# Kernel optimization log

Measured on AMD Instinct MI355X. Metric: run time of the kernel, lower is better.

Reference implementation:

```python
import jax, jax.numpy as jnp
import numpy as np

VOCAB_SIZE = 8192
DIM = 64


def setup_inputs() -> dict:
    key = jax.random.key(0)
    k1, k2 = jax.random.split(key)
    patches = jax.random.normal(k1, (16, 2048, DIM), dtype=jnp.float32)
    vocab = jax.random.normal(k2, (VOCAB_SIZE, DIM), dtype=jnp.float32)
    return {"patches": patches, "vocab": vocab}


def reference(patches, vocab):
    # torch.cdist(patches, vocab) -> [B, N, K] euclidean distances, then argmin over K.
    # argmin is invariant under sqrt, so compare squared distances:
    x2 = jnp.sum(patches * patches, axis=-1, keepdims=True)       # [B, N, 1]
    c2 = jnp.sum(vocab * vocab, axis=-1)                           # [K]
    xc = jnp.einsum("bnd,kd->bnk", patches, vocab)                # [B, N, K]
    d2 = x2 - 2.0 * xc + c2                                        # [B, N, K]
    tokens = jnp.argmin(d2, axis=-1)                               # [B, N] int
    return tokens
```

## Files before the change

### kernel.cpp

```cpp
#include <hip/hip_runtime.h>
#include <float.h>

#define VOCAB 8192
#define DIM 64
#define NQ 32768
#define CHUNK 64
#define THREADS 256
#define QPB 256
#define NSLICE 4

typedef __attribute__((ext_vector_type(8))) _Float16 half8;
typedef __attribute__((ext_vector_type(4))) float f32x4;

#define LO_SCALE 4096.0f
#define LO_INV   2.44140625e-4f

__global__ __launch_bounds__(256) void c2_kernel(const float* __restrict__ vocab,
                                                 float* __restrict__ c2h) {
    int c = blockIdx.x * 256 + threadIdx.x;
    const float4* row = (const float4*)(vocab + (size_t)c * DIM);
    float a0 = 0.f, a1 = 0.f, a2 = 0.f, a3 = 0.f;
#pragma unroll
    for (int k = 0; k < DIM / 4; ++k) {
        float4 v = row[k];
        a0 = fmaf(v.x, v.x, a0); a1 = fmaf(v.y, v.y, a1);
        a2 = fmaf(v.z, v.z, a2); a3 = fmaf(v.w, v.w, a3);
    }
    c2h[c] = -0.5f * ((a0 + a1) + (a2 + a3));
}

__global__ __launch_bounds__(256) void split_kernel(const float* __restrict__ src,
                                                    _Float16* __restrict__ hi,
                                                    _Float16* __restrict__ lo) {
    int t = blockIdx.x * 256 + threadIdx.x;
    const float4* s = (const float4*)(src + (size_t)t * 8);
    float4 f0 = s[0], f1 = s[1];
    float x[8] = {f0.x, f0.y, f0.z, f0.w, f1.x, f1.y, f1.z, f1.w};
    half8 h, l;
#pragma unroll
    for (int j = 0; j < 8; ++j) {
        _Float16 hh = (_Float16)x[j];
        h[j] = hh;
        l[j] = (_Float16)((x[j] - (float)hh) * LO_SCALE);
    }
    *(half8*)(hi + (size_t)t * 8) = h;
    *(half8*)(lo + (size_t)t * 8) = l;
}

__device__ __forceinline__ void gload_lds16(const void* g, void* lds_dst) {
    __builtin_amdgcn_global_load_lds(
        (const __attribute__((address_space(1))) void*)g,
        (__attribute__((address_space(3))) void*)lds_dst, 16, 0, 0);
}
__device__ __forceinline__ void gload_lds4(const void* g, void* lds_dst) {
    __builtin_amdgcn_global_load_lds(
        (const __attribute__((address_space(1))) void*)g,
        (__attribute__((address_space(3))) void*)lds_dst, 4, 0, 0);
}

__global__ __launch_bounds__(THREADS, 2)
void argmin_mfma(const float* __restrict__ patches,
                 const _Float16* __restrict__ vhi,
                 const _Float16* __restrict__ vlo,
                 const float* __restrict__ c2g,
                 float* __restrict__ ws_best,
                 int*   __restrict__ ws_idx) {
    constexpr int CSLICE = VOCAB / NSLICE;
    constexpr int NCHUNK = CSLICE / CHUNK;
    __shared__ __align__(16) char smem[2 * 16384 + 2 * 256];

    const int tid   = threadIdx.x;
    const int lane  = tid & 63;
    const int w     = tid >> 6;
    const int slice = blockIdx.x & (NSLICE - 1);
    const int qg    = blockIdx.x / NSLICE;
    const int qbase = qg * QPB + w * 64;
    const int cbase = slice * CSLICE;

    const int arow = lane & 15;
    const int akc  = lane >> 4;
    half8 Ah[4][2], Al[4][2];
#pragma unroll
    for (int t = 0; t < 4; ++t)
#pragma unroll
        for (int ks = 0; ks < 2; ++ks) {
            const float* p = patches + (size_t)(qbase + t * 16 + arow) * DIM
                           + ks * 32 + akc * 8;
            float4 f0 = *(const float4*)p;
            float4 f1 = *(const float4*)(p + 4);
            float x[8] = {f0.x, f0.y, f0.z, f0.w, f1.x, f1.y, f1.z, f1.w};
            half8 h, l;
#pragma unroll
            for (int j = 0; j < 8; ++j) {
                _Float16 hh = (_Float16)x[j];
                h[j] = hh;
                l[j] = (_Float16)((x[j] - (float)hh) * LO_SCALE);
            }
            Ah[t][ks] = h; Al[t][ks] = l;
        }

    const int s_srcoff = ((lane >> 3) * DIM) + (((lane & 7) ^ (lane >> 3)) * 8);
    const int fr = lane & 15;
    const int fx = fr & 7;
    const int b_off0 = fr * 128 + (((0 * 4 + akc) ^ fx) * 16);
    const int b_off1 = fr * 128 + (((1 * 4 + akc) ^ fx) * 16);

    auto stage = [&](int ch, int buf) {
        const size_t crow = (size_t)(cbase + ch * CHUNK) * DIM;
        char* dst = smem + buf * 16384;
#pragma unroll
        for (int j = 0; j < 2; ++j) {
            int r0 = (w + 4 * j) * 8;
            gload_lds16(vhi + crow + (size_t)r0 * DIM + s_srcoff, dst + r0 * 128);
            gload_lds16(vlo + crow + (size_t)r0 * DIM + s_srcoff, dst + 8192 + r0 * 128);
        }
        gload_lds4(c2g + cbase + ch * CHUNK + lane, smem + 32768 + buf * 256);
    };

    float best[4][4];
    int   bidx[4][4];
#pragma unroll
    for (int t = 0; t < 4; ++t)
#pragma unroll
        for (int j = 0; j < 4; ++j) { best[t][j] = -FLT_MAX; bidx[t][j] = 0; }

    stage(0, 0);

    for (int ch = 0; ch < NCHUNK; ++ch) {
        const int cur = ch & 1;
        if (ch + 1 < NCHUNK) {
            stage(ch + 1, cur ^ 1);
            asm volatile("s_waitcnt vmcnt(5)" ::: "memory");
        } else {
            asm volatile("s_waitcnt vmcnt(0)" ::: "memory");
        }
        __builtin_amdgcn_s_barrier();

        const char*  hib = smem + cur * 16384;
        const char*  lob = hib + 8192;
        const float* c2b = (const float*)(smem + 32768 + cur * 256);
        const int cb = cbase + ch * CHUNK;

#pragma unroll
        for (int nt = 0; nt < 4; ++nt) {
            const int rt = nt * 16;
            half8 Bh0 = *(const half8*)(hib + rt * 128 + b_off0);
            half8 Bh1 = *(const half8*)(hib + rt * 128 + b_off1);
            half8 Bl0 = *(const half8*)(lob + rt * 128 + b_off0);
            half8 Bl1 = *(const half8*)(lob + rt * 128 + b_off1);
            const float c2h = c2b[rt + fr];
            const int  cidx = cb + rt + fr;
            __builtin_amdgcn_s_setprio(1);
#pragma unroll
            for (int t = 0; t < 4; ++t) {
                f32x4 am = {c2h, c2h, c2h, c2h};
                f32x4 al = {0.f, 0.f, 0.f, 0.f};
                am = __builtin_amdgcn_mfma_f32_16x16x32_f16(Ah[t][0], Bh0, am, 0, 0, 0);
                am = __builtin_amdgcn_mfma_f32_16x16x32_f16(Ah[t][1], Bh1, am, 0, 0, 0);
                al = __builtin_amdgcn_mfma_f32_16x16x32_f16(Ah[t][0], Bl0, al, 0, 0, 0);
                al = __builtin_amdgcn_mfma_f32_16x16x32_f16(Ah[t][1], Bl1, al, 0, 0, 0);
                al = __builtin_amdgcn_mfma_f32_16x16x32_f16(Al[t][0], Bh0, al, 0, 0, 0);
                al = __builtin_amdgcn_mfma_f32_16x16x32_f16(Al[t][1], Bh1, al, 0, 0, 0);
#pragma unroll
                for (int j = 0; j < 4; ++j) {
                    float val = fmaf(al[j], LO_INV, am[j]);
                    if (val > best[t][j]) { best[t][j] = val; bidx[t][j] = cidx; }
                }
            }
            __builtin_amdgcn_s_setprio(0);
        }
        __builtin_amdgcn_s_barrier();
    }

#pragma unroll
    for (int t = 0; t < 4; ++t)
#pragma unroll
        for (int j = 0; j < 4; ++j) {
            float b = best[t][j]; int bi = bidx[t][j];
#pragma unroll
            for (int d = 1; d < 16; d <<= 1) {
                float ob = __shfl_xor(b, d, 64);
                int   oi = __shfl_xor(bi, d, 64);
                if (ob > b || (ob == b && oi < bi)) { b = ob; bi = oi; }
            }
            best[t][j] = b; bidx[t][j] = bi;
        }

    if ((lane & 15) == 0) {
        const int rg = lane >> 4;
#pragma unroll
        for (int t = 0; t < 4; ++t)
#pragma unroll
            for (int j = 0; j < 4; ++j) {
                int q = qbase + t * 16 + rg * 4 + j;
                ws_best[(size_t)slice * NQ + q] = best[t][j];
                ws_idx [(size_t)slice * NQ + q] = bidx[t][j];
            }
    }
}

__global__ __launch_bounds__(256) void merge_kernel(const float* __restrict__ ws_best,
                                                    const int* __restrict__ ws_idx,
                                                    int* __restrict__ out) {
    int q = blockIdx.x * 256 + threadIdx.x;
    float b = ws_best[q]; int bi = ws_idx[q];
#pragma unroll
    for (int s = 1; s < NSLICE; ++s) {
        float v = ws_best[(size_t)s * NQ + q];
        int  vi = ws_idx[(size_t)s * NQ + q];
        if (v > b || (v == b && vi < bi)) { b = v; bi = vi; }
    }
    out[q] = bi;
}

extern "C" void kernel_launch(void* const* d_in, const int* in_sizes, int n_in,
                              void* d_out, int out_size, void* d_ws, size_t ws_size,
                              hipStream_t stream) {
    const float* patches = (const float*)d_in[0];
    const float* vocab   = (const float*)d_in[1];
    char* ws = (char*)d_ws;
    float*    c2    = (float*)ws;
    _Float16* vhi   = (_Float16*)(ws + 32768);
    _Float16* vlo   = (_Float16*)(ws + 32768 + 1048576);
    float*    wbest = (float*)(ws + 32768 + 2097152);
    int*      widx  = (int*)  (ws + 32768 + 2097152 + 524288);
    int* out = (int*)d_out;

    c2_kernel   <<<VOCAB / 256, 256, 0, stream>>>(vocab, c2);
    split_kernel<<<(VOCAB * DIM / 8) / 256, 256, 0, stream>>>(vocab, vhi, vlo);
    argmin_mfma <<<(NQ / QPB) * NSLICE, THREADS, 0, stream>>>(patches, vhi, vlo, c2, wbest, widx);
    merge_kernel<<<NQ / 256, 256, 0, stream>>>(wbest, widx, out);
}
```

Measured before the change: 103.9 us.

## Switch distance GEMM to 32x32x16 MFMA tiles with new LDS layout

Replaces the 16x16x32 MFMA tiling with 32x32x16 MFMA, so each wave handles 32 queries against 32-codeword tiles. The LDS staging layout and read offsets change to feed the new B fragment shape. The argmin update now runs once per 16-element accumulator after the K loop. Queries per block drop from 256 to 128, which doubles the grid and the re-staging of the vocabulary across blocks. The per-block compare work and the cross-lane reduction widen to 32 lanes.

```diff
diff --git a/kernel.cpp b/kernel.cpp
--- a/kernel.cpp
+++ b/kernel.cpp
@@ -6,11 +6,11 @@
 #define NQ 32768
 #define CHUNK 64
 #define THREADS 256
-#define QPB 256
+#define QPB 128
 #define NSLICE 4
 
 typedef __attribute__((ext_vector_type(8))) _Float16 half8;
-typedef __attribute__((ext_vector_type(4))) float f32x4;
+typedef __attribute__((ext_vector_type(16))) float f32x16;
 
 #define LO_SCALE 4096.0f
 #define LO_INV   2.44140625e-4f
@@ -74,55 +74,53 @@
     const int w     = tid >> 6;
     const int slice = blockIdx.x & (NSLICE - 1);
     const int qg    = blockIdx.x / NSLICE;
-    const int qbase = qg * QPB + w * 64;
+    const int qbase = qg * QPB + w * 32;
     const int cbase = slice * CSLICE;
 
-    const int arow = lane & 15;
-    const int akc  = lane >> 4;
-    half8 Ah[4][2], Al[4][2];
-#pragma unroll
-    for (int t = 0; t < 4; ++t)
-#pragma unroll
-        for (int ks = 0; ks < 2; ++ks) {
-            const float* p = patches + (size_t)(qbase + t * 16 + arow) * DIM
-                           + ks * 32 + akc * 8;
-            float4 f0 = *(const float4*)p;
-            float4 f1 = *(const float4*)(p + 4);
-            float x[8] = {f0.x, f0.y, f0.z, f0.w, f1.x, f1.y, f1.z, f1.w};
-            half8 h, l;
-#pragma unroll
-            for (int j = 0; j < 8; ++j) {
-                _Float16 hh = (_Float16)x[j];
-                h[j] = hh;
-                l[j] = (_Float16)((x[j] - (float)hh) * LO_SCALE);
-            }
-            Ah[t][ks] = h; Al[t][ks] = l;
-        }
-
-    const int s_srcoff = ((lane >> 3) * DIM) + (((lane & 7) ^ (lane >> 3)) * 8);
-    const int fr = lane & 15;
-    const int fx = fr & 7;
-    const int b_off0 = fr * 128 + (((0 * 4 + akc) ^ fx) * 16);
-    const int b_off1 = fr * 128 + (((1 * 4 + akc) ^ fx) * 16);
+    const int col  = lane & 31;
+    const int ksel = lane >> 5;
+
+    half8 Ah[4], Al[4];
+#pragma unroll
+    for (int kk = 0; kk < 4; ++kk) {
+        const float* p = patches + (size_t)(qbase + col) * DIM + kk * 16 + ksel * 8;
+        float4 f0 = *(const float4*)p;
+        float4 f1 = *(const float4*)(p + 4);
+        float x[8] = {f0.x, f0.y, f0.z, f0.w, f1.x, f1.y, f1.z, f1.w};
+        half8 h, l;
+#pragma unroll
+        for (int j = 0; j < 8; ++j) {
+            _Float16 hh = (_Float16)x[j];
+            h[j] = hh;
+            l[j] = (_Float16)((x[j] - (float)hh) * LO_SCALE);
+        }
+        Ah[kk] = h; Al[kk] = l;
+    }
+
+    int soff[2];
+#pragma unroll
+    for (int j = 0; j < 2; ++j) {
+        int u = (4 * j + w) * 64 + lane;
+        int T = u >> 8, kk = (u >> 6) & 3, ks2 = (u >> 5) & 1, row = u & 31;
+        soff[j] = (T * 32 + row) * DIM + kk * 16 + ks2 * 8;
+    }
+    const int rdoff = ksel * 512 + col * 16;
 
     auto stage = [&](int ch, int buf) {
         const size_t crow = (size_t)(cbase + ch * CHUNK) * DIM;
         char* dst = smem + buf * 16384;
 #pragma unroll
         for (int j = 0; j < 2; ++j) {
-            int r0 = (w + 4 * j) * 8;
-            gload_lds16(vhi + crow + (size_t)r0 * DIM + s_srcoff, dst + r0 * 128);
-            gload_lds16(vlo + crow + (size_t)r0 * DIM + s_srcoff, dst + 8192 + r0 * 128);
+            gload_lds16(vhi + crow + soff[j], dst + (4 * j + w) * 1024);
+            gload_lds16(vlo + crow + soff[j], dst + 8192 + (4 * j + w) * 1024);
         }
         gload_lds4(c2g + cbase + ch * CHUNK + lane, smem + 32768 + buf * 256);
     };
 
-    float best[4][4];
-    int   bidx[4][4];
-#pragma unroll
-    for (int t = 0; t < 4; ++t)
-#pragma unroll
-        for (int j = 0; j < 4; ++j) { best[t][j] = -FLT_MAX; bidx[t][j] = 0; }
+    float best[16];
+    int   bidx[16];
+#pragma unroll
+    for (int r = 0; r < 16; ++r) { best[r] = -FLT_MAX; bidx[r] = 0; }
 
     stage(0, 0);
 
@@ -142,60 +140,57 @@
         const int cb = cbase + ch * CHUNK;
 
 #pragma unroll
-        for (int nt = 0; nt < 4; ++nt) {
-            const int rt = nt * 16;
-            half8 Bh0 = *(const half8*)(hib + rt * 128 + b_off0);
-            half8 Bh1 = *(const half8*)(hib + rt * 128 + b_off1);
-            half8 Bl0 = *(const half8*)(lob + rt * 128 + b_off0);
-            half8 Bl1 = *(const half8*)(lob + rt * 128 + b_off1);
-            const float c2h = c2b[rt + fr];
-            const int  cidx = cb + rt + fr;
+        for (int T = 0; T < 2; ++T) {
+            half8 Bh[4], Bl[4];
+#pragma unroll
+            for (int kk = 0; kk < 4; ++kk) {
+                Bh[kk] = *(const half8*)(hib + T * 4096 + kk * 1024 + rdoff);
+                Bl[kk] = *(const half8*)(lob + T * 4096 + kk * 1024 + rdoff);
+            }
+            const float c2h = c2b[T * 32 + col];
+            const int  cidx = cb + T * 32 + col;
+
+            f32x16 am, al;
+#pragma unroll
+            for (int r = 0; r < 16; ++r) { am[r] = c2h; al[r] = 0.f; }
+
             __builtin_amdgcn_s_setprio(1);
 #pragma unroll
-            for (int t = 0; t < 4; ++t) {
-                f32x4 am = {c2h, c2h, c2h, c2h};
-                f32x4 al = {0.f, 0.f, 0.f, 0.f};
-                am = __builtin_amdgcn_mfma_f32_16x16x32_f16(Ah[t][0], Bh0, am, 0, 0, 0);
-                am = __builtin_amdgcn_mfma_f32_16x16x32_f16(Ah[t][1], Bh1, am, 0, 0, 0);
-                al = __builtin_amdgcn_mfma_f32_16x16x32_f16(Ah[t][0], Bl0, al, 0, 0, 0);
-                al = __builtin_amdgcn_mfma_f32_16x16x32_f16(Ah[t][1], Bl1, al, 0, 0, 0);
-                al = __builtin_amdgcn_mfma_f32_16x16x32_f16(Al[t][0], Bh0, al, 0, 0, 0);
-                al = __builtin_amdgcn_mfma_f32_16x16x32_f16(Al[t][1], Bh1, al, 0, 0, 0);
-#pragma unroll
-                for (int j = 0; j < 4; ++j) {
-                    float val = fmaf(al[j], LO_INV, am[j]);
-                    if (val > best[t][j]) { best[t][j] = val; bidx[t][j] = cidx; }
-                }
+            for (int kk = 0; kk < 4; ++kk) {
+                am = __builtin_amdgcn_mfma_f32_32x32x16_f16(Ah[kk], Bh[kk], am, 0, 0, 0);
+                al = __builtin_amdgcn_mfma_f32_32x32x16_f16(Ah[kk], Bl[kk], al, 0, 0, 0);
+                al = __builtin_amdgcn_mfma_f32_32x32x16_f16(Al[kk], Bh[kk], al, 0, 0, 0);
             }
             __builtin_amdgcn_s_setprio(0);
+
+#pragma unroll
+            for (int r = 0; r < 16; ++r) {
+                float val = fmaf(al[r], LO_INV, am[r]);
+                if (val > best[r]) { best[r] = val; bidx[r] = cidx; }
+            }
         }
         __builtin_amdgcn_s_barrier();
     }
 
 #pragma unroll
-    for (int t = 0; t < 4; ++t)
-#pragma unroll
-        for (int j = 0; j < 4; ++j) {
-            float b = best[t][j]; int bi = bidx[t][j];
-#pragma unroll
-            for (int d = 1; d < 16; d <<= 1) {
-                float ob = __shfl_xor(b, d, 64);
-                int   oi = __shfl_xor(bi, d, 64);
-                if (ob > b || (ob == b && oi < bi)) { b = ob; bi = oi; }
-            }
-            best[t][j] = b; bidx[t][j] = bi;
-        }
-
-    if ((lane & 15) == 0) {
-        const int rg = lane >> 4;
-#pragma unroll
-        for (int t = 0; t < 4; ++t)
-#pragma unroll
-            for (int j = 0; j < 4; ++j) {
-                int q = qbase + t * 16 + rg * 4 + j;
-                ws_best[(size_t)slice * NQ + q] = best[t][j];
-                ws_idx [(size_t)slice * NQ + q] = bidx[t][j];
-            }
+    for (int r = 0; r < 16; ++r) {
+        float b = best[r]; int bi = bidx[r];
+#pragma unroll
+        for (int d = 1; d < 32; d <<= 1) {
+            float ob = __shfl_xor(b, d, 64);
+            int   oi = __shfl_xor(bi, d, 64);
+            if (ob > b || (ob == b && oi < bi)) { b = ob; bi = oi; }
+        }
+        best[r] = b; bidx[r] = bi;
+    }
+
+    if (col == 0) {
+#pragma unroll
+        for (int r = 0; r < 16; ++r) {
+            int q = qbase + (r & 3) + 8 * (r >> 2) + 4 * ksel;
+            ws_best[(size_t)slice * NQ + q] = best[r];
+            ws_idx [(size_t)slice * NQ + q] = bidx[r];
+        }
     }
 }
 
```

Result: slower. 139.3 us (+34.1%).

## Shrink per-wave query tile to 16 rows and raise occupancy to 3 blocks

Applied to the files above, without the earlier changes.

Each wave now processes one 16-query MFMA tile instead of four, so a block covers 64 queries and register usage drops. Launch bounds move to three blocks per CU to exploit the lower register pressure and increase parallelism. The trade-off is four times less reuse of each staged codebook chunk, so more blocks re-read vocab from global memory and LDS reads per MFMA increase.

```diff
diff --git a/kernel.cpp b/kernel.cpp
--- a/kernel.cpp
+++ b/kernel.cpp
@@ -6,7 +6,7 @@
 #define NQ 32768
 #define CHUNK 64
 #define THREADS 256
-#define QPB 256
+#define QPB 64
 #define NSLICE 4
 
 typedef __attribute__((ext_vector_type(8))) _Float16 half8;
@@ -58,7 +58,7 @@
         (__attribute__((address_space(3))) void*)lds_dst, 4, 0, 0);
 }
 
-__global__ __launch_bounds__(THREADS, 2)
+__global__ __launch_bounds__(THREADS, 3)
 void argmin_mfma(const float* __restrict__ patches,
                  const _Float16* __restrict__ vhi,
                  const _Float16* __restrict__ vlo,
@@ -74,30 +74,27 @@
     const int w     = tid >> 6;
     const int slice = blockIdx.x & (NSLICE - 1);
     const int qg    = blockIdx.x / NSLICE;
-    const int qbase = qg * QPB + w * 64;
+    const int qbase = qg * QPB + w * 16;
     const int cbase = slice * CSLICE;
 
     const int arow = lane & 15;
     const int akc  = lane >> 4;
-    half8 Ah[4][2], Al[4][2];
-#pragma unroll
-    for (int t = 0; t < 4; ++t)
-#pragma unroll
-        for (int ks = 0; ks < 2; ++ks) {
-            const float* p = patches + (size_t)(qbase + t * 16 + arow) * DIM
-                           + ks * 32 + akc * 8;
-            float4 f0 = *(const float4*)p;
-            float4 f1 = *(const float4*)(p + 4);
-            float x[8] = {f0.x, f0.y, f0.z, f0.w, f1.x, f1.y, f1.z, f1.w};
-            half8 h, l;
-#pragma unroll
-            for (int j = 0; j < 8; ++j) {
-                _Float16 hh = (_Float16)x[j];
-                h[j] = hh;
-                l[j] = (_Float16)((x[j] - (float)hh) * LO_SCALE);
-            }
-            Ah[t][ks] = h; Al[t][ks] = l;
-        }
+    half8 Ah[2], Al[2];
+#pragma unroll
+    for (int ks = 0; ks < 2; ++ks) {
+        const float* p = patches + (size_t)(qbase + arow) * DIM + ks * 32 + akc * 8;
+        float4 f0 = *(const float4*)p;
+        float4 f1 = *(const float4*)(p + 4);
+        float x[8] = {f0.x, f0.y, f0.z, f0.w, f1.x, f1.y, f1.z, f1.w};
+        half8 h, l;
+#pragma unroll
+        for (int j = 0; j < 8; ++j) {
+            _Float16 hh = (_Float16)x[j];
+            h[j] = hh;
+            l[j] = (_Float16)((x[j] - (float)hh) * LO_SCALE);
+        }
+        Ah[ks] = h; Al[ks] = l;
+    }
 
     const int s_srcoff = ((lane >> 3) * DIM) + (((lane & 7) ^ (lane >> 3)) * 8);
     const int fr = lane & 15;
@@ -117,12 +114,10 @@
         gload_lds4(c2g + cbase + ch * CHUNK + lane, smem + 32768 + buf * 256);
     };
 
-    float best[4][4];
-    int   bidx[4][4];
-#pragma unroll
-    for (int t = 0; t < 4; ++t)
-#pragma unroll
-        for (int j = 0; j < 4; ++j) { best[t][j] = -FLT_MAX; bidx[t][j] = 0; }
+    float best[4];
+    int   bidx[4];
+#pragma unroll
+    for (int j = 0; j < 4; ++j) { best[j] = -FLT_MAX; bidx[j] = 0; }
 
     stage(0, 0);
 
@@ -151,51 +146,44 @@
             const float c2h = c2b[rt + fr];
             const int  cidx = cb + rt + fr;
             __builtin_amdgcn_s_setprio(1);
-#pragma unroll
-            for (int t = 0; t < 4; ++t) {
-                f32x4 am = {c2h, c2h, c2h, c2h};
-                f32x4 al = {0.f, 0.f, 0.f, 0.f};
-                am = __builtin_amdgcn_mfma_f32_16x16x32_f16(Ah[t][0], Bh0, am, 0, 0, 0);
-                am = __builtin_amdgcn_mfma_f32_16x16x32_f16(Ah[t][1], Bh1, am, 0, 0, 0);
-                al = __builtin_amdgcn_mfma_f32_16x16x32_f16(Ah[t][0], Bl0, al, 0, 0, 0);
-                al = __builtin_amdgcn_mfma_f32_16x16x32_f16(Ah[t][1], Bl1, al, 0, 0, 0);
-                al = __builtin_amdgcn_mfma_f32_16x16x32_f16(Al[t][0], Bh0, al, 0, 0, 0);
-                al = __builtin_amdgcn_mfma_f32_16x16x32_f16(Al[t][1], Bh1, al, 0, 0, 0);
-#pragma unroll
-                for (int j = 0; j < 4; ++j) {
-                    float val = fmaf(al[j], LO_INV, am[j]);
-                    if (val > best[t][j]) { best[t][j] = val; bidx[t][j] = cidx; }
-                }
+            f32x4 am = {c2h, c2h, c2h, c2h};
+            f32x4 al = {0.f, 0.f, 0.f, 0.f};
+            am = __builtin_amdgcn_mfma_f32_16x16x32_f16(Ah[0], Bh0, am, 0, 0, 0);
+            am = __builtin_amdgcn_mfma_f32_16x16x32_f16(Ah[1], Bh1, am, 0, 0, 0);
+            al = __builtin_amdgcn_mfma_f32_16x16x32_f16(Ah[0], Bl0, al, 0, 0, 0);
+            al = __builtin_amdgcn_mfma_f32_16x16x32_f16(Ah[1], Bl1, al, 0, 0, 0);
+            al = __builtin_amdgcn_mfma_f32_16x16x32_f16(Al[0], Bh0, al, 0, 0, 0);
+            al = __builtin_amdgcn_mfma_f32_16x16x32_f16(Al[1], Bh1, al, 0, 0, 0);
+            __builtin_amdgcn_s_setprio(0);
+#pragma unroll
+            for (int j = 0; j < 4; ++j) {
+                float val = fmaf(al[j], LO_INV, am[j]);
+                if (val > best[j]) { best[j] = val; bidx[j] = cidx; }
             }
-            __builtin_amdgcn_s_setprio(0);
         }
         __builtin_amdgcn_s_barrier();
     }
 
 #pragma unroll
-    for (int t = 0; t < 4; ++t)
-#pragma unroll
-        for (int j = 0; j < 4; ++j) {
-            float b = best[t][j]; int bi = bidx[t][j];
-#pragma unroll
-            for (int d = 1; d < 16; d <<= 1) {
-                float ob = __shfl_xor(b, d, 64);
-                int   oi = __shfl_xor(bi, d, 64);
-                if (ob > b || (ob == b && oi < bi)) { b = ob; bi = oi; }
-            }
-            best[t][j] = b; bidx[t][j] = bi;
-        }
+    for (int j = 0; j < 4; ++j) {
+        float b = best[j]; int bi = bidx[j];
+#pragma unroll
+        for (int d = 1; d < 16; d <<= 1) {
+            float ob = __shfl_xor(b, d, 64);
+            int   oi = __shfl_xor(bi, d, 64);
+            if (ob > b || (ob == b && oi < bi)) { b = ob; bi = oi; }
+        }
+        best[j] = b; bidx[j] = bi;
+    }
 
     if ((lane & 15) == 0) {
         const int rg = lane >> 4;
 #pragma unroll
-        for (int t = 0; t < 4; ++t)
-#pragma unroll
-            for (int j = 0; j < 4; ++j) {
-                int q = qbase + t * 16 + rg * 4 + j;
-                ws_best[(size_t)slice * NQ + q] = best[t][j];
-                ws_idx [(size_t)slice * NQ + q] = bidx[t][j];
-            }
+        for (int j = 0; j < 4; ++j) {
+            int q = qbase + rg * 4 + j;
+            ws_best[(size_t)slice * NQ + q] = best[j];
+            ws_idx [(size_t)slice * NQ + q] = bidx[j];
+        }
     }
 }
 
```

Measured after the change: 128.4 us. 1.24x slower.
